# Optimization experiments

Measured on AMD Instinct MI355X. Metric: run time of the kernel, lower is better.

## Reference

```python
import jax, jax.numpy as jnp
import numpy as np

B, N, D, K = 4, 2048, 128, 32
EPS = 1e-5  # nn.LayerNorm default eps


def _lin(k, fan_in, fan_out):
    kw, kb = jax.random.split(k)
    s = 1.0 / np.sqrt(fan_in)
    w = jax.random.uniform(kw, (fan_in, fan_out), jnp.float32, -s, s)
    b = jax.random.uniform(kb, (fan_out,), jnp.float32, -s, s)
    return w, b


def setup_inputs() -> dict:
    key = jax.random.key(0)
    ks = jax.random.split(key, 3)
    inp = {}
    inp["features"] = jax.random.normal(ks[0], (B, N, D), jnp.float32)
    inp["coords"] = jax.random.uniform(ks[1], (B, N, 3), jnp.float32) * 64.0
    names = [("ql", D, D), ("kl", D, D), ("vl", D, D), ("pl1", 3, D), ("pl2", D, D),
             ("we1", D, D), ("we2", D, D), ("pe1", 3, D), ("pe2", D, D),
             ("sg1", D, D), ("sg2", D, D)]
    k2 = jax.random.split(ks[2], len(names))
    for (nm, fi, fo), kk in zip(names, k2):
        w, b = _lin(kk, fi, fo)
        inp[nm + "_w"] = w
        inp[nm + "_b"] = b
    inp["lnA_g"] = jnp.ones((D,), jnp.float32)
    inp["lnA_b"] = jnp.zeros((D,), jnp.float32)
    inp["lnF_g"] = jnp.ones((D,), jnp.float32)
    inp["lnF_b"] = jnp.zeros((D,), jnp.float32)
    return inp


def _sparsemax_k(z):
    # sparsemax over axis=1 (the K neighbor axis) of [N, K, D]
    zs = -jnp.sort(-z, axis=1)                      # descending sort
    zc = jnp.cumsum(zs, axis=1)
    r = jnp.arange(1, K + 1, dtype=z.dtype)[None, :, None]
    support = (r * zs) > (zc - 1.0)
    kz = jnp.sum(support, axis=1, keepdims=True).astype(jnp.int32)  # >= 1
    tau = (jnp.take_along_axis(zc, kz - 1, axis=1) - 1.0) / kz.astype(z.dtype)
    return jnp.maximum(z - tau, 0.0)


def _sg_prop(x, src, tgt, n):
    # SGConv (K=1) propagation: D^{-1/2}(A+I)D^{-1/2} x with self-loops added
    ar = jnp.arange(n)
    s = jnp.concatenate([src, ar])
    t = jnp.concatenate([tgt, ar])
    deg = jax.ops.segment_sum(jnp.ones(s.shape, x.dtype), t, num_segments=n)
    dinv = jax.lax.rsqrt(deg)
    norm = dinv[s] * dinv[t]
    return jax.ops.segment_sum(x[s] * norm[:, None], t, num_segments=n)


def reference(features, coords,
              ql_w, ql_b, kl_w, kl_b, vl_w, vl_b,
              pl1_w, pl1_b, pl2_w, pl2_b,
              we1_w, we1_b, we2_w, we2_b,
              lnA_g, lnA_b,
              pe1_w, pe1_b, pe2_w, pe2_b,
              sg1_w, sg1_b, sg2_w, sg2_b,
              lnF_g, lnF_b):
    def ln(x, g, b):
        m = jnp.mean(x, axis=-1, keepdims=True)
        v = jnp.var(x, axis=-1, keepdims=True)
        return (x - m) * jax.lax.rsqrt(v + EPS) * g + b

    def one(feat, coord):
        # ---- RNSA: KNN self-attention with positional embedding ----
        d2 = jnp.sum((coord[:, None, :] - coord[None, :, :]) ** 2, axis=-1)  # [N,N]
        _, idx = jax.lax.top_k(-d2, K)                   # [N,K], self included first
        diff = coord[idx] - coord[:, None, :]            # [N,K,3]
        fc = jnp.maximum(diff @ pl1_w + pl1_b, 0.0) @ pl2_w + pl2_b  # [N,K,D]
        pe = fc + feat[idx]
        Q = jnp.maximum(feat @ ql_w + ql_b, 0.0)         # [N,D]
        Kf = jnp.maximum(pe @ kl_w + kl_b, 0.0)          # [N,K,D]
        V = pe @ vl_w + vl_b
        rel = (Kf - Q[:, None, :]) * fc
        w = jnp.maximum(rel @ we1_w + we1_b, 0.0) @ we2_w + we2_b
        w = _sparsemax_k(w)                              # attn_drop is identity (eval)
        x_att = feat + jnp.einsum('nkd,nkd->nd', V, w)   # residual add
        cf = jnp.maximum(coord @ pe1_w + pe1_b, 0.0) @ pe2_w + pe2_b
        x_in = ln(x_att, lnA_g, lnA_b)
        x_pe = x_in + cf
        d2m = d2 + jnp.where(jnp.eye(N, dtype=bool), jnp.inf, 0.0)  # knn_graph: loop=False
        _, idx2 = jax.lax.top_k(-d2m, K)                 # [N,K] neighbors (sources)
        src = idx2.reshape(-1)
        tgt = jnp.repeat(jnp.arange(N), K)
        h = _sg_prop(x_pe, src, tgt, N) @ sg1_w + sg1_b
        h = jnp.maximum(h, 0.0)
        h = _sg_prop(h, src, tgt, N) @ sg2_w + sg2_b     # dropout is identity (eval)
        return ln(h + x_in, lnF_g, lnF_b)

    return jax.vmap(one)(features, coords)
```

## Files before the change

kernel.cpp:

```cpp
#include <hip/hip_runtime.h>
#include <hip/hip_bf16.h>


namespace {
constexpr int BB = 4;
constexpr int NN = 2048;
constexpr int DD = 128;
constexpr int KK = 32;
constexpr float LNEPS = 1e-5f;
constexpr int SH = 136;

constexpr int W_QL = 0, W_KL = 16384, W_VL = 32768, W_PL2 = 49152, W_WE1 = 65536,
              W_WE2 = 81920, W_PE2 = 98304, W_SG1 = 114688, W_SG2 = 131072,
              W_PL1 = 147456, W_PE1 = 147840,
              B_QL = 148224, B_KL = 148352, B_VL = 148480, B_PL1 = 148608, B_PL2 = 148736,
              B_WE1 = 148864, B_WE2 = 148992, B_PE1 = 149120, B_PE2 = 149248,
              B_SG1 = 149376, B_SG2 = 149504,
              LNA_G = 149632, LNA_B = 149760, LNF_G = 149888, LNF_B = 150016;

constexpr long OFF_FEAT  = 0;
constexpr long OFF_Q     = 1l << 20;
constexpr long OFF_XATT  = 2l << 20;
constexpr long OFF_XIN   = 3l << 20;
constexpr long OFF_XPE   = 4l << 20;
constexpr long OFF_H1    = 5l << 20;
constexpr long OFF_COORD = 6l << 20;
constexpr long OFF_W     = (6l << 20) + 32768;
constexpr long OFF_IDX   = (6l << 20) + 262144;
}

typedef __attribute__((ext_vector_type(8))) short short8;
typedef __attribute__((ext_vector_type(4))) float f32x4;

struct WPtrs { const void* p[26]; };

__device__ __forceinline__ unsigned short f2bf(float f) {
  unsigned u = __float_as_uint(f);
  return (unsigned short)((u + 0x7fffu + ((u >> 16) & 1u)) >> 16);
}
__device__ __forceinline__ float bf2f(unsigned short h) {
  return __uint_as_float(((unsigned)h) << 16);
}
__device__ __forceinline__ f32x4 mfma16(short8 a, short8 b, f32x4 c) {
  return __builtin_amdgcn_mfma_f32_16x16x32_bf16(a, b, c, 0, 0, 0);
}

__global__ void k_detect(const unsigned* __restrict__ lnAg, int* __restrict__ flag) {
  if (threadIdx.x == 0 && blockIdx.x == 0) *flag = ((lnAg[0] & 0xFFFFu) != 0u) ? 1 : 0;
}

__global__ __launch_bounds__(256) void k_convert_inputs(
    const void* __restrict__ feat, const void* __restrict__ coord, const int* __restrict__ flag,
    float* __restrict__ featf, float* __restrict__ coordf) {
  const bool isbf = (*flag != 0);
  const int nf = BB * NN * DD, nc = BB * NN * 3;
  for (int i = blockIdx.x * 256 + threadIdx.x; i < nf + nc; i += gridDim.x * 256) {
    if (i < nf) {
      featf[i] = isbf ? __bfloat162float(((const __hip_bfloat16*)feat)[i])
                      : ((const float*)feat)[i];
    } else {
      const int j = i - nf;
      coordf[j] = isbf ? __bfloat162float(((const __hip_bfloat16*)coord)[j])
                       : ((const float*)coord)[j];
    }
  }
}

__global__ __launch_bounds__(256) void k_convert_weights(WPtrs wp, const int* __restrict__ flag,
                                                         float* __restrict__ Wf) {
  const int sizes[26] = {16384,16384,16384,16384,16384,16384,16384,16384,16384,
                         384,384,
                         128,128,128,128,128,128,128,128,128,128,128,
                         128,128,128,128};
  const int offs[26] = {W_QL,W_KL,W_VL,W_PL2,W_WE1,W_WE2,W_PE2,W_SG1,W_SG2,
                        W_PL1,W_PE1,
                        B_QL,B_KL,B_VL,B_PL1,B_PL2,B_WE1,B_WE2,B_PE1,B_PE2,B_SG1,B_SG2,
                        LNA_G,LNA_B,LNF_G,LNF_B};
  const bool isbf = (*flag != 0);
  const int t = blockIdx.x;
  float* dst = Wf + offs[t];
  const int n = sizes[t];
  if (isbf) {
    const __hip_bfloat16* src = (const __hip_bfloat16*)wp.p[t];
    for (int i = threadIdx.x; i < n; i += 256) dst[i] = __bfloat162float(src[i]);
  } else {
    const float* src = (const float*)wp.p[t];
    for (int i = threadIdx.x; i < n; i += 256) dst[i] = src[i];
  }
}

__global__ __launch_bounds__(256) void k_pack(const float* __restrict__ Wf,
                                              unsigned short* __restrict__ pkH,
                                              unsigned short* __restrict__ pkL) {
  const int woffs[5] = {W_PL2, W_KL, W_VL, W_WE1, W_WE2};
  const int m = blockIdx.x;
  const float* W = Wf + woffs[m];
  unsigned short* H = pkH + m * 16384;
  unsigned short* L = pkL + m * 16384;
  for (int f = threadIdx.x; f < 16384; f += 256) {
    const int j = f & 7, lane = (f >> 3) & 63, ks = (f >> 9) & 3, nt = f >> 11;
    const int k = ks * 32 + ((lane >> 4) << 3) + j, n = nt * 16 + (lane & 15);
    const float v = W[k * 128 + n];
    const unsigned short h = f2bf(v);
    H[f] = h;
    L[f] = f2bf(v - bf2f(h));
  }
}

__global__ __launch_bounds__(256) void k_knn(const float* __restrict__ coordf,
                                             int* __restrict__ idx1, int* __restrict__ idx2) {
  __shared__ float cs[NN * 3];
  __shared__ int tops[4][33];
  const int tid = threadIdx.x;
  const int wv = tid >> 6, lane = tid & 63;
  const int blk = blockIdx.x;
  const int b = blk >> 9;
  const int i = ((blk & 511) << 2) + wv;
  const float* cb = coordf + (long)b * NN * 3;
  for (int t = tid; t < NN * 3 / 4; t += 256) ((float4*)cs)[t] = ((const float4*)cb)[t];
  __syncthreads();
  const float qx = cs[i*3+0], qy = cs[i*3+1], qz = cs[i*3+2];
  float v[32];
  unsigned removed = 0u;
  float bv = 1e30f; int bj = 0x7fffffff;
  #pragma unroll
  for (int m = 0; m < 32; m++) {
    const int j = m * 64 + lane;
    const float dx = cs[j*3+0] - qx, dy = cs[j*3+1] - qy, dz = cs[j*3+2] - qz;
    const float d2 = __fadd_rn(__fadd_rn(__fmul_rn(dx,dx), __fmul_rn(dy,dy)), __fmul_rn(dz,dz));
    v[m] = d2;
    if (d2 < bv) { bv = d2; bj = j; }
  }
  for (int s = 0; s < 33; s++) {
    float mv = bv; int mj = bj;
    #pragma unroll
    for (int off = 1; off < 64; off <<= 1) {
      const float ov = __shfl_xor(mv, off, 64);
      const int   oj = __shfl_xor(mj, off, 64);
      if (ov < mv || (ov == mv && oj < mj)) { mv = ov; mj = oj; }
    }
    if (lane == 0) tops[wv][s] = mj;
    if ((mj & 63) == lane) {
      removed |= 1u << (mj >> 6);
      bv = 1e30f; bj = 0x7fffffff;
      #pragma unroll
      for (int m = 0; m < 32; m++) {
        if (!((removed >> m) & 1u) && v[m] < bv) { bv = v[m]; bj = m * 64 + lane; }
      }
    }
  }
  const unsigned long long sm = __ballot(lane < 33 && tops[wv][lane] == i);
  const int p = sm ? (__ffsll((long long)sm) - 1) : 32;
  if (lane < KK) {
    const long g = (long)b * NN + i;
    idx1[g * KK + lane] = tops[wv][lane];
    idx2[g * KK + lane] = tops[wv][lane + (lane >= p ? 1 : 0)];
  }
}

__global__ __launch_bounds__(256) void k_rowgemm(const float* __restrict__ X, float* __restrict__ Y,
                                                 const float* __restrict__ Wf, int woff, int boff, int dorelu) {
  __shared__ float xs[2][DD];
  const int tid = threadIdx.x; const int rr = tid >> 7, d = tid & 127;
  const long row = (long)blockIdx.x * 2 + rr;
  xs[rr][d] = X[row * DD + d];
  __syncthreads();
  const float* Wm = Wf + woff;
  float acc = Wf[boff + d];
  for (int c = 0; c < DD; c++) acc = fmaf(xs[rr][c], Wm[c * DD + d], acc);
  if (dorelu) acc = fmaxf(acc, 0.f);
  Y[row * DD + d] = acc;
}

__device__ __forceinline__ void mm_core(const unsigned short* sH, const unsigned short* sL,
                                        const unsigned short* __restrict__ wH,
                                        const unsigned short* __restrict__ wL,
                                        bool useLoB, int lane, int wv, f32x4 acc[2][2]) {
  const int colq = lane & 15, quad = lane >> 4;
  #pragma unroll
  for (int mt = 0; mt < 2; ++mt) {
    const int arow = mt * 16 + colq;
    f32x4 a0 = {0.f, 0.f, 0.f, 0.f}, a1 = {0.f, 0.f, 0.f, 0.f};
    #pragma unroll
    for (int ks = 0; ks < 4; ++ks) {
      const short8 ah = *(const short8*)(sH + arow * SH + ks * 32 + quad * 8);
      const short8 al = *(const short8*)(sL + arow * SH + ks * 32 + quad * 8);
      const int nt0 = 2 * wv, nt1 = 2 * wv + 1;
      const short8 b0 = *(const short8*)(wH + ((nt0 * 4 + ks) * 64 + lane) * 8);
      const short8 b1 = *(const short8*)(wH + ((nt1 * 4 + ks) * 64 + lane) * 8);
      a0 = mfma16(ah, b0, a0);
      a0 = mfma16(al, b0, a0);
      a1 = mfma16(ah, b1, a1);
      a1 = mfma16(al, b1, a1);
      if (useLoB) {
        const short8 bl0 = *(const short8*)(wL + ((nt0 * 4 + ks) * 64 + lane) * 8);
        const short8 bl1 = *(const short8*)(wL + ((nt1 * 4 + ks) * 64 + lane) * 8);
        a0 = mfma16(ah, bl0, a0);
        a1 = mfma16(ah, bl1, a1);
      }
    }
    acc[mt][0] = a0;
    acc[mt][1] = a1;
  }
}

__device__ __forceinline__ void split_store2(unsigned short* H, unsigned short* L,
                                             int row0, int col, float v0, float v1) {
  float2 vv; vv.x = v0; vv.y = v1;
  const __hip_bfloat162 h2 = __float22bfloat162_rn(vv);
  float2 ll; ll.x = v0 - __bfloat162float(h2.x); ll.y = v1 - __bfloat162float(h2.y);
  const __hip_bfloat162 l2 = __float22bfloat162_rn(ll);
  *(__hip_bfloat16*)(H + row0 * SH + col) = h2.x;
  *(__hip_bfloat16*)(H + (row0 + 1) * SH + col) = h2.y;
  *(__hip_bfloat16*)(L + row0 * SH + col) = l2.x;
  *(__hip_bfloat16*)(L + (row0 + 1) * SH + col) = l2.y;
}

__global__ __launch_bounds__(256, 2) void k_attn(const float* __restrict__ featf,
                                              const float* __restrict__ coordf,
                                              const float* __restrict__ Qm,
                                              const int* __restrict__ idx1,
                                              const float* __restrict__ Wf,
                                              const unsigned short* __restrict__ pkH,
                                              const unsigned short* __restrict__ pkL,
                                              const int* __restrict__ flag,
                                              float* __restrict__ x_att) {
  __shared__ __align__(16) unsigned short AH[KK*SH], AL[KK*SH], CH[KK*SH], CL[KK*SH];
  __shared__ int nb[KK];
  const int tid = threadIdx.x;
  const int lane = tid & 63, wv = tid >> 6;
  const int colq = lane & 15, quad = lane >> 4;
  const int g = blockIdx.x; const int i = g & (NN - 1); const int b = g >> 11;
  const long bN = (long)b * NN;
  const bool useLoB = (*flag == 0);
  if (tid < KK) nb[tid] = idx1[(long)g * KK + tid];
  __syncthreads();
  const int row8 = tid >> 3, c0 = (tid & 7) * 16;

  {
    const float* cb = coordf + (long)b * NN * 3;
    const int j = nb[row8];
    const float dx = cb[j*3+0] - cb[i*3+0], dy = cb[j*3+1] - cb[i*3+1], dz = cb[j*3+2] - cb[i*3+2];
    #pragma unroll
    for (int h2 = 0; h2 < 2; ++h2) {
      short8 oh, ol;
      #pragma unroll
      for (int c4 = 0; c4 < 2; ++c4) {
        const int cc = c0 + h2*8 + c4*4;
        const float4 w0 = *(const float4*)(Wf + W_PL1 + cc);
        const float4 w1 = *(const float4*)(Wf + W_PL1 + 128 + cc);
        const float4 w2 = *(const float4*)(Wf + W_PL1 + 256 + cc);
        const float4 bp = *(const float4*)(Wf + B_PL1 + cc);
        const float vv[4] = {
          fmaxf(fmaf(dz,w2.x,fmaf(dy,w1.x,fmaf(dx,w0.x,bp.x))), 0.f),
          fmaxf(fmaf(dz,w2.y,fmaf(dy,w1.y,fmaf(dx,w0.y,bp.y))), 0.f),
          fmaxf(fmaf(dz,w2.z,fmaf(dy,w1.z,fmaf(dx,w0.z,bp.z))), 0.f),
          fmaxf(fmaf(dz,w2.w,fmaf(dy,w1.w,fmaf(dx,w0.w,bp.w))), 0.f)};
        #pragma unroll
        for (int e = 0; e < 4; ++e) {
          const unsigned short h = f2bf(vv[e]);
          oh[c4*4+e] = (short)h;
          ol[c4*4+e] = (short)f2bf(vv[e] - bf2f(h));
        }
      }
      *(short8*)(AH + row8*SH + c0 + h2*8) = oh;
      *(short8*)(AL + row8*SH + c0 + h2*8) = ol;
    }
  }
  __syncthreads();
  f32x4 acc[2][2];
  float fc[2][2][4];
  {
    mm_core(AH, AL, pkH + 0*16384, pkL + 0*16384, useLoB, lane, wv, acc);
    #pragma unroll
    for (int ntl = 0; ntl < 2; ++ntl) {
      const int col = (2*wv + ntl)*16 + colq;
      const float bv = Wf[B_PL2 + col];
      #pragma unroll
      for (int mt = 0; mt < 2; ++mt) {
        const int rowb = mt*16 + quad*4;
        float pe[4];
        #pragma unroll
        for (int r = 0; r < 4; ++r) {
          const float f = acc[mt][ntl][r] + bv;
          fc[mt][ntl][r] = f;
          pe[r] = f + featf[(bN + nb[rowb + r]) * DD + col];
        }
        split_store2(CH, CL, rowb + 0, col, pe[0], pe[1]);
        split_store2(CH, CL, rowb + 2, col, pe[2], pe[3]);
      }
    }
  }
  __syncthreads();
  {
    mm_core(CH, CL, pkH + 1*16384, pkL + 1*16384, useLoB, lane, wv, acc);
    #pragma unroll
    for (int ntl = 0; ntl < 2; ++ntl) {
      const int col = (2*wv + ntl)*16 + colq;
      const float bv = Wf[B_KL + col];
      const float qv = Qm[(bN + i) * DD + col];
      #pragma unroll
      for (int mt = 0; mt < 2; ++mt) {
        const int rowb = mt*16 + quad*4;
        float rel[4];
        #pragma unroll
        for (int r = 0; r < 4; ++r) {
          const float kf = fmaxf(acc[mt][ntl][r] + bv, 0.f);
          rel[r] = (kf - qv) * fc[mt][ntl][r];
        }
        split_store2(AH, AL, rowb + 0, col, rel[0], rel[1]);
        split_store2(AH, AL, rowb + 2, col, rel[2], rel[3]);
      }
    }
  }
  f32x4 Vacc[2][2];
  mm_core(CH, CL, pkH + 2*16384, pkL + 2*16384, useLoB, lane, wv, Vacc);
  __syncthreads();
  {
    mm_core(AH, AL, pkH + 3*16384, pkL + 3*16384, useLoB, lane, wv, acc);
    #pragma unroll
    for (int ntl = 0; ntl < 2; ++ntl) {
      const int col = (2*wv + ntl)*16 + colq;
      const float bv = Wf[B_WE1 + col];
      #pragma unroll
      for (int mt = 0; mt < 2; ++mt) {
        const int rowb = mt*16 + quad*4;
        split_store2(CH, CL, rowb + 0, col,
                     fmaxf(acc[mt][ntl][0] + bv, 0.f), fmaxf(acc[mt][ntl][1] + bv, 0.f));
        split_store2(CH, CL, rowb + 2, col,
                     fmaxf(acc[mt][ntl][2] + bv, 0.f), fmaxf(acc[mt][ntl][3] + bv, 0.f));
      }
    }
  }
  __syncthreads();
  f32x4 Wacc[2][2];
  mm_core(CH, CL, pkH + 4*16384, pkL + 4*16384, useLoB, lane, wv, Wacc);

  #pragma unroll
  for (int ntl = 0; ntl < 2; ++ntl) {
    const int col = (2*wv + ntl)*16 + colq;
    const float bw = Wf[B_WE2 + col];
    const float bvv = Wf[B_VL + col];
    float z[8], Vv[8];
    #pragma unroll
    for (int mt = 0; mt < 2; ++mt)
      #pragma unroll
      for (int r = 0; r < 4; ++r) {
        z[mt*4+r]  = Wacc[mt][ntl][r] + bw;
        Vv[mt*4+r] = Vacc[mt][ntl][r] + bvv;
      }
    float S = 0.f;
    #pragma unroll
    for (int e = 0; e < 8; ++e) S += z[e];
    S += __shfl_xor(S, 16, 64); S += __shfl_xor(S, 32, 64);
    float tau = (S - 1.0f) * (1.0f / 32.0f);
    int cnt = 32;
    for (int it = 0; it < 40; ++it) {
      float s = 0.f; int c = 0;
      #pragma unroll
      for (int e = 0; e < 8; ++e) { if (z[e] > tau) { s += z[e]; c++; } }
      s += __shfl_xor(s, 16, 64); s += __shfl_xor(s, 32, 64);
      c += __shfl_xor(c, 16, 64); c += __shfl_xor(c, 32, 64);
      const float ntau = (s - 1.0f) / (float)c;
      const int changed = (c != cnt);
      cnt = c; tau = ntau;
      if (!__any(changed)) break;
    }
    float pv = 0.f;
    #pragma unroll
    for (int e = 0; e < 8; ++e) pv = fmaf(fmaxf(z[e] - tau, 0.f), Vv[e], pv);
    pv += __shfl_xor(pv, 16, 64); pv += __shfl_xor(pv, 32, 64);
    if (quad == 0) x_att[(bN + i) * DD + col] = featf[(bN + i) * DD + col] + pv;
  }
}

__global__ __launch_bounds__(256) void k_lnA_pe(const float* __restrict__ x_att,
                                                const float* __restrict__ coordf,
                                                const float* __restrict__ Wf,
                                                float* __restrict__ x_in, float* __restrict__ x_pe) {
  __shared__ float xs[2][DD];
  __shared__ float ts[2][DD];
  const int tid = threadIdx.x; const int rr = tid >> 7, d = tid & 127;
  const long g = (long)blockIdx.x * 2 + rr;
  const int i = (int)(g & (NN - 1)); const int b = (int)(g >> 11);
  const float* cb = coordf + (long)b * NN * 3;
  const float cx = cb[i*3+0], cy = cb[i*3+1], cz = cb[i*3+2];
  const float xa = x_att[g * DD + d];
  xs[rr][d] = xa;
  const float* w1 = Wf + W_PE1;
  const float t = Wf[B_PE1 + d] + cx * w1[d] + cy * w1[128 + d] + cz * w1[256 + d];
  ts[rr][d] = fmaxf(t, 0.f);
  __syncthreads();
  float sm = 0.f, s2 = 0.f;
  for (int c = 0; c < DD; c++) { const float x = xs[rr][c]; sm += x; s2 = fmaf(x, x, s2); }
  const float m = sm * (1.f/128.f);
  const float var = s2 * (1.f/128.f) - m * m;
  float cf = Wf[B_PE2 + d];
  const float* w2 = Wf + W_PE2;
  for (int c = 0; c < DD; c++) cf = fmaf(ts[rr][c], w2[c * DD + d], cf);
  const float xin = (xa - m) * rsqrtf(var + LNEPS) * Wf[LNA_G + d] + Wf[LNA_B + d];
  x_in[g * DD + d] = xin;
  x_pe[g * DD + d] = xin + cf;
}

__global__ __launch_bounds__(256) void k_sg1(const float* __restrict__ x_pe,
                                             const int* __restrict__ idx2,
                                             const float* __restrict__ Wf, float* __restrict__ h1) {
  __shared__ float gs[2][DD];
  __shared__ int nb[2][KK];
  const int tid = threadIdx.x; const int rr = tid >> 7, d = tid & 127;
  const long g = (long)blockIdx.x * 2 + rr;
  const int b = (int)(g >> 11); const long bN = (long)b * NN;
  if (tid < 64) nb[tid >> 5][tid & 31] = idx2[((long)blockIdx.x * 2 + (tid >> 5)) * KK + (tid & 31)];
  __syncthreads();
  float s = x_pe[g * DD + d];
  for (int k = 0; k < KK; k++) s += x_pe[(bN + nb[rr][k]) * DD + d];
  gs[rr][d] = s * (1.f / 33.f);
  __syncthreads();
  float acc = Wf[B_SG1 + d];
  const float* w = Wf + W_SG1;
  for (int c = 0; c < DD; c++) acc = fmaf(gs[rr][c], w[c * DD + d], acc);
  h1[g * DD + d] = fmaxf(acc, 0.f);
}

__global__ __launch_bounds__(256) void k_sg2(const float* __restrict__ h1,
                                             const int* __restrict__ idx2,
                                             const float* __restrict__ x_in,
                                             const float* __restrict__ Wf,
                                             const int* __restrict__ flag,
                                             void* __restrict__ out) {
  __shared__ float gs[2][DD];
  __shared__ float ys[2][DD];
  __shared__ int nb[2][KK];
  const int tid = threadIdx.x; const int rr = tid >> 7, d = tid & 127;
  const long g = (long)blockIdx.x * 2 + rr;
  const int b = (int)(g >> 11); const long bN = (long)b * NN;
  if (tid < 64) nb[tid >> 5][tid & 31] = idx2[((long)blockIdx.x * 2 + (tid >> 5)) * KK + (tid & 31)];
  __syncthreads();
  float s = h1[g * DD + d];
  for (int k = 0; k < KK; k++) s += h1[(bN + nb[rr][k]) * DD + d];
  gs[rr][d] = s * (1.f / 33.f);
  __syncthreads();
  float acc = Wf[B_SG2 + d];
  const float* w = Wf + W_SG2;
  for (int c = 0; c < DD; c++) acc = fmaf(gs[rr][c], w[c * DD + d], acc);
  const float y = acc + x_in[g * DD + d];
  ys[rr][d] = y;
  __syncthreads();
  float sm = 0.f, s2 = 0.f;
  for (int c = 0; c < DD; c++) { const float x = ys[rr][c]; sm += x; s2 = fmaf(x, x, s2); }
  const float m = sm * (1.f/128.f);
  const float var = s2 * (1.f/128.f) - m * m;
  const float o = (y - m) * rsqrtf(var + LNEPS) * Wf[LNF_G + d] + Wf[LNF_B + d];
  if (*flag) ((__hip_bfloat16*)out)[g * DD + d] = __float2bfloat16(o);
  else       ((float*)out)[g * DD + d] = o;
}

extern "C" void kernel_launch(void* const* d_in, const int* in_sizes, int n_in,
                              void* d_out, int out_size, void* d_ws, size_t ws_size,
                              hipStream_t stream) {
  float* ws = (float*)d_ws;
  float* featf  = ws + OFF_FEAT;
  float* Qb     = ws + OFF_Q;
  float* x_att  = ws + OFF_XATT;
  float* x_in   = ws + OFF_XIN;
  float* x_pe   = ws + OFF_XPE;
  float* h1     = ws + OFF_H1;
  float* coordf = ws + OFF_COORD;
  float* Wf     = ws + OFF_W;
  int* idx1 = (int*)(ws + OFF_IDX);
  int* idx2 = idx1 + (long)BB * NN * KK;
  int* flag = idx2 + (long)BB * NN * KK;
  unsigned short* pkH = (unsigned short*)(flag + 64);
  unsigned short* pkL = pkH + 5 * 16384;

  WPtrs wp;
  const int map[26] = {2,4,6,10,12,14,18,20,22, 8,16,
                       3,5,7,9,11,13,15,17,19,21,23,
                       24,25,26,27};
  for (int t = 0; t < 26; t++) wp.p[t] = d_in[map[t]];

  k_detect<<<1, 64, 0, stream>>>((const unsigned*)d_in[24], flag);
  k_convert_inputs<<<2048, 256, 0, stream>>>(d_in[0], d_in[1], flag, featf, coordf);
  k_convert_weights<<<26, 256, 0, stream>>>(wp, flag, Wf);
  k_pack<<<5, 256, 0, stream>>>(Wf, pkH, pkL);
  k_knn<<<BB * NN / 4, 256, 0, stream>>>(coordf, idx1, idx2);
  k_rowgemm<<<BB * NN / 2, 256, 0, stream>>>(featf, Qb, Wf, W_QL, B_QL, 1);
  k_attn<<<BB * NN, 256, 0, stream>>>(featf, coordf, Qb, idx1, Wf, pkH, pkL, flag, x_att);
  k_lnA_pe<<<BB * NN / 2, 256, 0, stream>>>(x_att, coordf, Wf, x_in, x_pe);
  k_sg1<<<BB * NN / 2, 256, 0, stream>>>(x_pe, idx2, Wf, h1);
  k_sg2<<<BB * NN / 2, 256, 0, stream>>>(h1, idx2, x_in, Wf, flag, (void*)d_out);
}
```

Baseline: 541.3 us.

## Move post-attention GEMMs to split-bf16 MFMA tiles and fuse Q projection into attention

The three per-row scalar GEMM kernels (positional-embedding second layer, both SGConv linears) become 32-row tiles that use the existing split-bf16 hi/lo MFMA core with pre-packed weights. This removes the scalar fp32 FMA loops that reread weights for every pair of rows. The separate Q row-GEMM kernel is dropped, and Q is now computed inside the attention block from the feature row staged in shared memory. LayerNorms switch to 8-lane shuffle reductions and neighbour gathers use float4 loads, at the cost of more weight packing and the precision of the split-bf16 path.

```diff
diff --git a/kernel.cpp b/kernel.cpp
--- a/kernel.cpp
+++ b/kernel.cpp
@@ -9,6 +9,7 @@
 constexpr int KK = 32;
 constexpr float LNEPS = 1e-5f;
 constexpr int SH = 136;
+constexpr int SF = 132;
 
 constexpr int W_QL = 0, W_KL = 16384, W_VL = 32768, W_PL2 = 49152, W_WE1 = 65536,
               W_WE2 = 81920, W_PE2 = 98304, W_SG1 = 114688, W_SG2 = 131072,
@@ -19,7 +20,6 @@
               LNA_G = 149632, LNA_B = 149760, LNF_G = 149888, LNF_B = 150016;
 
 constexpr long OFF_FEAT  = 0;
-constexpr long OFF_Q     = 1l << 20;
 constexpr long OFF_XATT  = 2l << 20;
 constexpr long OFF_XIN   = 3l << 20;
 constexpr long OFF_XPE   = 4l << 20;
@@ -92,7 +92,7 @@
 __global__ __launch_bounds__(256) void k_pack(const float* __restrict__ Wf,
                                               unsigned short* __restrict__ pkH,
                                               unsigned short* __restrict__ pkL) {
-  const int woffs[5] = {W_PL2, W_KL, W_VL, W_WE1, W_WE2};
+  const int woffs[8] = {W_PL2, W_KL, W_VL, W_WE1, W_WE2, W_PE2, W_SG1, W_SG2};
   const int m = blockIdx.x;
   const float* W = Wf + woffs[m];
   unsigned short* H = pkH + m * 16384;
@@ -156,20 +156,6 @@
     idx1[g * KK + lane] = tops[wv][lane];
     idx2[g * KK + lane] = tops[wv][lane + (lane >= p ? 1 : 0)];
   }
-}
-
-__global__ __launch_bounds__(256) void k_rowgemm(const float* __restrict__ X, float* __restrict__ Y,
-                                                 const float* __restrict__ Wf, int woff, int boff, int dorelu) {
-  __shared__ float xs[2][DD];
-  const int tid = threadIdx.x; const int rr = tid >> 7, d = tid & 127;
-  const long row = (long)blockIdx.x * 2 + rr;
-  xs[rr][d] = X[row * DD + d];
-  __syncthreads();
-  const float* Wm = Wf + woff;
-  float acc = Wf[boff + d];
-  for (int c = 0; c < DD; c++) acc = fmaf(xs[rr][c], Wm[c * DD + d], acc);
-  if (dorelu) acc = fmaxf(acc, 0.f);
-  Y[row * DD + d] = acc;
 }
 
 __device__ __forceinline__ void mm_core(const unsigned short* sH, const unsigned short* sL,
@@ -216,9 +202,24 @@
   *(__hip_bfloat16*)(L + (row0 + 1) * SH + col) = l2.y;
 }
 
+__device__ __forceinline__ void split_store_row16(unsigned short* H, unsigned short* L,
+                                                  int row, int c0, const float* v) {
+  #pragma unroll
+  for (int h2 = 0; h2 < 2; ++h2) {
+    short8 oh, ol;
+    #pragma unroll
+    for (int e = 0; e < 8; ++e) {
+      const float x = v[h2 * 8 + e];
+      const unsigned short h = f2bf(x);
+      oh[e] = (short)h; ol[e] = (short)f2bf(x - bf2f(h));
+    }
+    *(short8*)(H + row * SH + c0 + h2 * 8) = oh;
+    *(short8*)(L + row * SH + c0 + h2 * 8) = ol;
+  }
+}
+
 __global__ __launch_bounds__(256, 2) void k_attn(const float* __restrict__ featf,
                                               const float* __restrict__ coordf,
-                                              const float* __restrict__ Qm,
                                               const int* __restrict__ idx1,
                                               const float* __restrict__ Wf,
                                               const unsigned short* __restrict__ pkH,
@@ -227,6 +228,8 @@
                                               float* __restrict__ x_att) {
   __shared__ __align__(16) unsigned short AH[KK*SH], AL[KK*SH], CH[KK*SH], CL[KK*SH];
   __shared__ int nb[KK];
+  __shared__ float Fs[DD];
+  __shared__ float Qs[DD];
   const int tid = threadIdx.x;
   const int lane = tid & 63, wv = tid >> 6;
   const int colq = lane & 15, quad = lane >> 4;
@@ -234,38 +237,36 @@
   const long bN = (long)b * NN;
   const bool useLoB = (*flag == 0);
   if (tid < KK) nb[tid] = idx1[(long)g * KK + tid];
+  if (tid < DD) Fs[tid] = featf[(bN + i) * DD + tid];
   __syncthreads();
   const int row8 = tid >> 3, c0 = (tid & 7) * 16;
 
+  {
+    const int dq = tid >> 1, half = tid & 1;
+    float q = 0.f;
+    const float* wq = Wf + W_QL + dq;
+    for (int c = half * 64; c < half * 64 + 64; ++c) q = fmaf(Fs[c], wq[c * DD], q);
+    q += __shfl_xor(q, 1, 64);
+    if (half == 0) Qs[dq] = fmaxf(q + Wf[B_QL + dq], 0.f);
+  }
   {
     const float* cb = coordf + (long)b * NN * 3;
     const int j = nb[row8];
     const float dx = cb[j*3+0] - cb[i*3+0], dy = cb[j*3+1] - cb[i*3+1], dz = cb[j*3+2] - cb[i*3+2];
-    #pragma unroll
-    for (int h2 = 0; h2 < 2; ++h2) {
-      short8 oh, ol;
-      #pragma unroll
-      for (int c4 = 0; c4 < 2; ++c4) {
-        const int cc = c0 + h2*8 + c4*4;
-        const float4 w0 = *(const float4*)(Wf + W_PL1 + cc);
-        const float4 w1 = *(const float4*)(Wf + W_PL1 + 128 + cc);
-        const float4 w2 = *(const float4*)(Wf + W_PL1 + 256 + cc);
-        const float4 bp = *(const float4*)(Wf + B_PL1 + cc);
-        const float vv[4] = {
-          fmaxf(fmaf(dz,w2.x,fmaf(dy,w1.x,fmaf(dx,w0.x,bp.x))), 0.f),
-          fmaxf(fmaf(dz,w2.y,fmaf(dy,w1.y,fmaf(dx,w0.y,bp.y))), 0.f),
-          fmaxf(fmaf(dz,w2.z,fmaf(dy,w1.z,fmaf(dx,w0.z,bp.z))), 0.f),
-          fmaxf(fmaf(dz,w2.w,fmaf(dy,w1.w,fmaf(dx,w0.w,bp.w))), 0.f)};
-        #pragma unroll
-        for (int e = 0; e < 4; ++e) {
-          const unsigned short h = f2bf(vv[e]);
-          oh[c4*4+e] = (short)h;
-          ol[c4*4+e] = (short)f2bf(vv[e] - bf2f(h));
-        }
-      }
-      *(short8*)(AH + row8*SH + c0 + h2*8) = oh;
-      *(short8*)(AL + row8*SH + c0 + h2*8) = ol;
-    }
+    float t1v[16];
+    #pragma unroll
+    for (int c4 = 0; c4 < 4; ++c4) {
+      const int cc = c0 + c4*4;
+      const float4 w0 = *(const float4*)(Wf + W_PL1 + cc);
+      const float4 w1 = *(const float4*)(Wf + W_PL1 + 128 + cc);
+      const float4 w2 = *(const float4*)(Wf + W_PL1 + 256 + cc);
+      const float4 bp = *(const float4*)(Wf + B_PL1 + cc);
+      t1v[c4*4+0] = fmaxf(fmaf(dz,w2.x,fmaf(dy,w1.x,fmaf(dx,w0.x,bp.x))), 0.f);
+      t1v[c4*4+1] = fmaxf(fmaf(dz,w2.y,fmaf(dy,w1.y,fmaf(dx,w0.y,bp.y))), 0.f);
+      t1v[c4*4+2] = fmaxf(fmaf(dz,w2.z,fmaf(dy,w1.z,fmaf(dx,w0.z,bp.z))), 0.f);
+      t1v[c4*4+3] = fmaxf(fmaf(dz,w2.w,fmaf(dy,w1.w,fmaf(dx,w0.w,bp.w))), 0.f);
+    }
+    split_store_row16(AH, AL, row8, c0, t1v);
   }
   __syncthreads();
   f32x4 acc[2][2];
@@ -298,7 +299,7 @@
     for (int ntl = 0; ntl < 2; ++ntl) {
       const int col = (2*wv + ntl)*16 + colq;
       const float bv = Wf[B_KL + col];
-      const float qv = Qm[(bN + i) * DD + col];
+      const float qv = Qs[col];
       #pragma unroll
       for (int mt = 0; mt < 2; ++mt) {
         const int rowb = mt*16 + quad*4;
@@ -370,90 +371,229 @@
     #pragma unroll
     for (int e = 0; e < 8; ++e) pv = fmaf(fmaxf(z[e] - tau, 0.f), Vv[e], pv);
     pv += __shfl_xor(pv, 16, 64); pv += __shfl_xor(pv, 32, 64);
-    if (quad == 0) x_att[(bN + i) * DD + col] = featf[(bN + i) * DD + col] + pv;
+    if (quad == 0) x_att[(bN + i) * DD + col] = Fs[col] + pv;
   }
 }
 
 __global__ __launch_bounds__(256) void k_lnA_pe(const float* __restrict__ x_att,
                                                 const float* __restrict__ coordf,
                                                 const float* __restrict__ Wf,
+                                                const unsigned short* __restrict__ pkH,
+                                                const unsigned short* __restrict__ pkL,
+                                                const int* __restrict__ flag,
                                                 float* __restrict__ x_in, float* __restrict__ x_pe) {
-  __shared__ float xs[2][DD];
-  __shared__ float ts[2][DD];
-  const int tid = threadIdx.x; const int rr = tid >> 7, d = tid & 127;
-  const long g = (long)blockIdx.x * 2 + rr;
-  const int i = (int)(g & (NN - 1)); const int b = (int)(g >> 11);
-  const float* cb = coordf + (long)b * NN * 3;
-  const float cx = cb[i*3+0], cy = cb[i*3+1], cz = cb[i*3+2];
-  const float xa = x_att[g * DD + d];
-  xs[rr][d] = xa;
-  const float* w1 = Wf + W_PE1;
-  const float t = Wf[B_PE1 + d] + cx * w1[d] + cy * w1[128 + d] + cz * w1[256 + d];
-  ts[rr][d] = fmaxf(t, 0.f);
-  __syncthreads();
+  __shared__ __align__(16) unsigned short AH[KK*SH], AL[KK*SH];
+  __shared__ float Xf[KK][SF];
+  const int tid = threadIdx.x;
+  const int lane = tid & 63, wv = tid >> 6;
+  const int colq = lane & 15, quad = lane >> 4;
+  const bool useLoB = (*flag == 0);
+  const int row8 = tid >> 3, c0 = (tid & 7) * 16;
+  const long gg0 = (long)blockIdx.x * 32;
+  const long gr = gg0 + row8;
+  const int b = (int)(gr >> 11), i = (int)(gr & (NN - 1));
+
+  float xa[16];
+  {
+    const float* xr = x_att + gr * DD + c0;
+    #pragma unroll
+    for (int e = 0; e < 16; e += 4) {
+      const float4 v = *(const float4*)(xr + e);
+      xa[e] = v.x; xa[e+1] = v.y; xa[e+2] = v.z; xa[e+3] = v.w;
+    }
+  }
   float sm = 0.f, s2 = 0.f;
-  for (int c = 0; c < DD; c++) { const float x = xs[rr][c]; sm += x; s2 = fmaf(x, x, s2); }
+  #pragma unroll
+  for (int e = 0; e < 16; ++e) { sm += xa[e]; s2 = fmaf(xa[e], xa[e], s2); }
+  #pragma unroll
+  for (int off = 1; off < 8; off <<= 1) {
+    sm += __shfl_xor(sm, off, 64);
+    s2 += __shfl_xor(s2, off, 64);
+  }
   const float m = sm * (1.f/128.f);
   const float var = s2 * (1.f/128.f) - m * m;
-  float cf = Wf[B_PE2 + d];
-  const float* w2 = Wf + W_PE2;
-  for (int c = 0; c < DD; c++) cf = fmaf(ts[rr][c], w2[c * DD + d], cf);
-  const float xin = (xa - m) * rsqrtf(var + LNEPS) * Wf[LNA_G + d] + Wf[LNA_B + d];
-  x_in[g * DD + d] = xin;
-  x_pe[g * DD + d] = xin + cf;
+  const float rstd = rsqrtf(var + LNEPS);
+  float xin[16];
+  #pragma unroll
+  for (int e = 0; e < 16; ++e) {
+    xin[e] = (xa[e] - m) * rstd * Wf[LNA_G + c0 + e] + Wf[LNA_B + c0 + e];
+    Xf[row8][c0 + e] = xin[e];
+  }
+  #pragma unroll
+  for (int e = 0; e < 16; e += 4) {
+    float4 v; v.x = xin[e]; v.y = xin[e+1]; v.z = xin[e+2]; v.w = xin[e+3];
+    *(float4*)(x_in + gr * DD + c0 + e) = v;
+  }
+  {
+    const float* cp = coordf + ((long)b * NN + i) * 3;
+    const float cx = cp[0], cy = cp[1], cz = cp[2];
+    float tv[16];
+    #pragma unroll
+    for (int c4 = 0; c4 < 4; ++c4) {
+      const int cc = c0 + c4*4;
+      const float4 w0 = *(const float4*)(Wf + W_PE1 + cc);
+      const float4 w1 = *(const float4*)(Wf + W_PE1 + 128 + cc);
+      const float4 w2 = *(const float4*)(Wf + W_PE1 + 256 + cc);
+      const float4 bp = *(const float4*)(Wf + B_PE1 + cc);
+      tv[c4*4+0] = fmaxf(fmaf(cz,w2.x,fmaf(cy,w1.x,fmaf(cx,w0.x,bp.x))), 0.f);
+      tv[c4*4+1] = fmaxf(fmaf(cz,w2.y,fmaf(cy,w1.y,fmaf(cx,w0.y,bp.y))), 0.f);
+      tv[c4*4+2] = fmaxf(fmaf(cz,w2.z,fmaf(cy,w1.z,fmaf(cx,w0.z,bp.z))), 0.f);
+      tv[c4*4+3] = fmaxf(fmaf(cz,w2.w,fmaf(cy,w1.w,fmaf(cx,w0.w,bp.w))), 0.f);
+    }
+    split_store_row16(AH, AL, row8, c0, tv);
+  }
+  __syncthreads();
+  f32x4 acc[2][2];
+  mm_core(AH, AL, pkH + 5*16384, pkL + 5*16384, useLoB, lane, wv, acc);
+  #pragma unroll
+  for (int ntl = 0; ntl < 2; ++ntl) {
+    const int col = (2*wv + ntl)*16 + colq;
+    const float bv = Wf[B_PE2 + col];
+    #pragma unroll
+    for (int mt = 0; mt < 2; ++mt) {
+      const int rowb = mt*16 + quad*4;
+      #pragma unroll
+      for (int r = 0; r < 4; ++r)
+        x_pe[(gg0 + rowb + r) * DD + col] = Xf[rowb + r][col] + acc[mt][ntl][r] + bv;
+    }
+  }
 }
 
 __global__ __launch_bounds__(256) void k_sg1(const float* __restrict__ x_pe,
                                              const int* __restrict__ idx2,
-                                             const float* __restrict__ Wf, float* __restrict__ h1) {
-  __shared__ float gs[2][DD];
-  __shared__ int nb[2][KK];
-  const int tid = threadIdx.x; const int rr = tid >> 7, d = tid & 127;
-  const long g = (long)blockIdx.x * 2 + rr;
-  const int b = (int)(g >> 11); const long bN = (long)b * NN;
-  if (tid < 64) nb[tid >> 5][tid & 31] = idx2[((long)blockIdx.x * 2 + (tid >> 5)) * KK + (tid & 31)];
-  __syncthreads();
-  float s = x_pe[g * DD + d];
-  for (int k = 0; k < KK; k++) s += x_pe[(bN + nb[rr][k]) * DD + d];
-  gs[rr][d] = s * (1.f / 33.f);
-  __syncthreads();
-  float acc = Wf[B_SG1 + d];
-  const float* w = Wf + W_SG1;
-  for (int c = 0; c < DD; c++) acc = fmaf(gs[rr][c], w[c * DD + d], acc);
-  h1[g * DD + d] = fmaxf(acc, 0.f);
+                                             const float* __restrict__ Wf,
+                                             const unsigned short* __restrict__ pkH,
+                                             const unsigned short* __restrict__ pkL,
+                                             const int* __restrict__ flag,
+                                             float* __restrict__ h1) {
+  __shared__ __align__(16) unsigned short AH[KK*SH], AL[KK*SH];
+  __shared__ int nb2[32][KK];
+  const int tid = threadIdx.x;
+  const int lane = tid & 63, wv = tid >> 6;
+  const int colq = lane & 15, quad = lane >> 4;
+  const bool useLoB = (*flag == 0);
+  const int row8 = tid >> 3, c0 = (tid & 7) * 16;
+  const long gg0 = (long)blockIdx.x * 32;
+  const long bN = (gg0 >> 11) << 11;
+  for (int t = tid; t < 32 * KK; t += 256)
+    nb2[t >> 5][t & 31] = idx2[(gg0 + (t >> 5)) * KK + (t & 31)];
+  __syncthreads();
+  float s[16];
+  {
+    const float* sp = x_pe + (gg0 + row8) * DD + c0;
+    #pragma unroll
+    for (int e = 0; e < 16; e += 4) {
+      const float4 v = *(const float4*)(sp + e);
+      s[e] = v.x; s[e+1] = v.y; s[e+2] = v.z; s[e+3] = v.w;
+    }
+  }
+  for (int k = 0; k < KK; ++k) {
+    const float* np_ = x_pe + (bN + nb2[row8][k]) * DD + c0;
+    #pragma unroll
+    for (int e = 0; e < 16; e += 4) {
+      const float4 v = *(const float4*)(np_ + e);
+      s[e] += v.x; s[e+1] += v.y; s[e+2] += v.z; s[e+3] += v.w;
+    }
+  }
+  #pragma unroll
+  for (int e = 0; e < 16; ++e) s[e] *= (1.f / 33.f);
+  split_store_row16(AH, AL, row8, c0, s);
+  __syncthreads();
+  f32x4 acc[2][2];
+  mm_core(AH, AL, pkH + 6*16384, pkL + 6*16384, useLoB, lane, wv, acc);
+  #pragma unroll
+  for (int ntl = 0; ntl < 2; ++ntl) {
+    const int col = (2*wv + ntl)*16 + colq;
+    const float bv = Wf[B_SG1 + col];
+    #pragma unroll
+    for (int mt = 0; mt < 2; ++mt) {
+      const int rowb = mt*16 + quad*4;
+      #pragma unroll
+      for (int r = 0; r < 4; ++r)
+        h1[(gg0 + rowb + r) * DD + col] = fmaxf(acc[mt][ntl][r] + bv, 0.f);
+    }
+  }
 }
 
 __global__ __launch_bounds__(256) void k_sg2(const float* __restrict__ h1,
                                              const int* __restrict__ idx2,
                                              const float* __restrict__ x_in,
                                              const float* __restrict__ Wf,
+                                             const unsigned short* __restrict__ pkH,
+                                             const unsigned short* __restrict__ pkL,
                                              const int* __restrict__ flag,
                                              void* __restrict__ out) {
-  __shared__ float gs[2][DD];
-  __shared__ float ys[2][DD];
-  __shared__ int nb[2][KK];
-  const int tid = threadIdx.x; const int rr = tid >> 7, d = tid & 127;
-  const long g = (long)blockIdx.x * 2 + rr;
-  const int b = (int)(g >> 11); const long bN = (long)b * NN;
-  if (tid < 64) nb[tid >> 5][tid & 31] = idx2[((long)blockIdx.x * 2 + (tid >> 5)) * KK + (tid & 31)];
-  __syncthreads();
-  float s = h1[g * DD + d];
-  for (int k = 0; k < KK; k++) s += h1[(bN + nb[rr][k]) * DD + d];
-  gs[rr][d] = s * (1.f / 33.f);
-  __syncthreads();
-  float acc = Wf[B_SG2 + d];
-  const float* w = Wf + W_SG2;
-  for (int c = 0; c < DD; c++) acc = fmaf(gs[rr][c], w[c * DD + d], acc);
-  const float y = acc + x_in[g * DD + d];
-  ys[rr][d] = y;
-  __syncthreads();
+  __shared__ __align__(16) unsigned short AH[KK*SH], AL[KK*SH];
+  __shared__ float Yf[KK][SF];
+  __shared__ int nb2[32][KK];
+  const int tid = threadIdx.x;
+  const int lane = tid & 63, wv = tid >> 6;
+  const int colq = lane & 15, quad = lane >> 4;
+  const bool isbf = (*flag != 0);
+  const bool useLoB = !isbf;
+  const int row8 = tid >> 3, c0 = (tid & 7) * 16;
+  const long gg0 = (long)blockIdx.x * 32;
+  const long bN = (gg0 >> 11) << 11;
+  for (int t = tid; t < 32 * KK; t += 256)
+    nb2[t >> 5][t & 31] = idx2[(gg0 + (t >> 5)) * KK + (t & 31)];
+  __syncthreads();
+  float s[16];
+  {
+    const float* sp = h1 + (gg0 + row8) * DD + c0;
+    #pragma unroll
+    for (int e = 0; e < 16; e += 4) {
+      const float4 v = *(const float4*)(sp + e);
+      s[e] = v.x; s[e+1] = v.y; s[e+2] = v.z; s[e+3] = v.w;
+    }
+  }
+  for (int k = 0; k < KK; ++k) {
+    const float* np_ = h1 + (bN + nb2[row8][k]) * DD + c0;
+    #pragma unroll
+    for (int e = 0; e < 16; e += 4) {
+      const float4 v = *(const float4*)(np_ + e);
+      s[e] += v.x; s[e+1] += v.y; s[e+2] += v.z; s[e+3] += v.w;
+    }
+  }
+  #pragma unroll
+  for (int e = 0; e < 16; ++e) s[e] *= (1.f / 33.f);
+  split_store_row16(AH, AL, row8, c0, s);
+  __syncthreads();
+  f32x4 acc[2][2];
+  mm_core(AH, AL, pkH + 7*16384, pkL + 7*16384, useLoB, lane, wv, acc);
+  #pragma unroll
+  for (int ntl = 0; ntl < 2; ++ntl) {
+    const int col = (2*wv + ntl)*16 + colq;
+    const float bv = Wf[B_SG2 + col];
+    #pragma unroll
+    for (int mt = 0; mt < 2; ++mt) {
+      const int rowb = mt*16 + quad*4;
+      #pragma unroll
+      for (int r = 0; r < 4; ++r)
+        Yf[rowb + r][col] = acc[mt][ntl][r] + bv + x_in[(gg0 + rowb + r) * DD + col];
+    }
+  }
+  __syncthreads();
+  float y[16];
+  #pragma unroll
+  for (int e = 0; e < 16; ++e) y[e] = Yf[row8][c0 + e];
   float sm = 0.f, s2 = 0.f;
-  for (int c = 0; c < DD; c++) { const float x = ys[rr][c]; sm += x; s2 = fmaf(x, x, s2); }
+  #pragma unroll
+  for (int e = 0; e < 16; ++e) { sm += y[e]; s2 = fmaf(y[e], y[e], s2); }
+  #pragma unroll
+  for (int off = 1; off < 8; off <<= 1) {
+    sm += __shfl_xor(sm, off, 64);
+    s2 += __shfl_xor(s2, off, 64);
+  }
   const float m = sm * (1.f/128.f);
   const float var = s2 * (1.f/128.f) - m * m;
-  const float o = (y - m) * rsqrtf(var + LNEPS) * Wf[LNF_G + d] + Wf[LNF_B + d];
-  if (*flag) ((__hip_bfloat16*)out)[g * DD + d] = __float2bfloat16(o);
-  else       ((float*)out)[g * DD + d] = o;
+  const float rstd = rsqrtf(var + LNEPS);
+  const long gr = gg0 + row8;
+  #pragma unroll
+  for (int e = 0; e < 16; ++e) {
+    const float o = (y[e] - m) * rstd * Wf[LNF_G + c0 + e] + Wf[LNF_B + c0 + e];
+    if (isbf) ((__hip_bfloat16*)out)[gr * DD + c0 + e] = __float2bfloat16(o);
+    else      ((float*)out)[gr * DD + c0 + e] = o;
+  }
 }
 
 extern "C" void kernel_launch(void* const* d_in, const int* in_sizes, int n_in,
@@ -461,7 +601,6 @@
                               hipStream_t stream) {
   float* ws = (float*)d_ws;
   float* featf  = ws + OFF_FEAT;
-  float* Qb     = ws + OFF_Q;
   float* x_att  = ws + OFF_XATT;
   float* x_in   = ws + OFF_XIN;
   float* x_pe   = ws + OFF_XPE;
@@ -472,7 +611,7 @@
   int* idx2 = idx1 + (long)BB * NN * KK;
   int* flag = idx2 + (long)BB * NN * KK;
   unsigned short* pkH = (unsigned short*)(flag + 64);
-  unsigned short* pkL = pkH + 5 * 16384;
+  unsigned short* pkL = pkH + 8 * 16384;
 
   WPtrs wp;
   const int map[26] = {2,4,6,10,12,14,18,20,22, 8,16,
@@ -483,11 +622,10 @@
   k_detect<<<1, 64, 0, stream>>>((const unsigned*)d_in[24], flag);
   k_convert_inputs<<<2048, 256, 0, stream>>>(d_in[0], d_in[1], flag, featf, coordf);
   k_convert_weights<<<26, 256, 0, stream>>>(wp, flag, Wf);
-  k_pack<<<5, 256, 0, stream>>>(Wf, pkH, pkL);
+  k_pack<<<8, 256, 0, stream>>>(Wf, pkH, pkL);
   k_knn<<<BB * NN / 4, 256, 0, stream>>>(coordf, idx1, idx2);
-  k_rowgemm<<<BB * NN / 2, 256, 0, stream>>>(featf, Qb, Wf, W_QL, B_QL, 1);
-  k_attn<<<BB * NN, 256, 0, stream>>>(featf, coordf, Qb, idx1, Wf, pkH, pkL, flag, x_att);
-  k_lnA_pe<<<BB * NN / 2, 256, 0, stream>>>(x_att, coordf, Wf, x_in, x_pe);
-  k_sg1<<<BB * NN / 2, 256, 0, stream>>>(x_pe, idx2, Wf, h1);
-  k_sg2<<<BB * NN / 2, 256, 0, stream>>>(h1, idx2, x_in, Wf, flag, (void*)d_out);
-}
+  k_attn<<<BB * NN, 256, 0, stream>>>(featf, coordf, idx1, Wf, pkH, pkL, flag, x_att);
+  k_lnA_pe<<<BB * NN / 32, 256, 0, stream>>>(x_att, coordf, Wf, pkH, pkL, flag, x_in, x_pe);
+  k_sg1<<<BB * NN / 32, 256, 0, stream>>>(x_pe, idx2, Wf, pkH, pkL, flag, h1);
+  k_sg2<<<BB * NN / 32, 256, 0, stream>>>(h1, idx2, x_in, Wf, pkH, pkL, flag, (void*)d_out);
+}
```

Measured after the change: 556.6 us. +2.8%, slower.
